# Optimization experiments

Measured on AMD Instinct MI355X. Metric: run time of the kernel, lower is better.

## Reference

```python
import jax, jax.numpy as jnp
import numpy as np

DIM = 512; NH = 8; AG = 144; WIN = 18; PS = 12; B = 128; N0 = 320


def _pool_matrix(in_size, out_size):
    # PyTorch AdaptiveAvgPool2d window rule: start=floor(i*in/out), end=ceil((i+1)*in/out)
    P = np.zeros((out_size, in_size), np.float32)
    for i in range(out_size):
        s = (i * in_size) // out_size
        e = -((-(i + 1) * in_size) // out_size)
        P[i, s:e] = 1.0 / (e - s)
    return jnp.asarray(P)


def setup_inputs() -> dict:
    key = jax.random.key(0)
    ks = jax.random.split(key, 12)
    std = 0.02
    return {
        "x": jax.random.normal(ks[0], (B, N0, DIM), jnp.float32),
        "qkv_w": jax.random.normal(ks[1], (DIM, 3 * DIM), jnp.float32) * 0.02,
        "proj_w": jax.random.normal(ks[2], (DIM, DIM), jnp.float32) * 0.02,
        "proj_b": jnp.zeros((DIM,), jnp.float32),
        "dwc_w": jax.random.normal(ks[3], (DIM, 1, 3, 3), jnp.float32) * 0.1,
        "dwc_b": jnp.zeros((DIM,), jnp.float32),
        "an_bias": jax.random.normal(ks[4], (NH, AG, 7, 7), jnp.float32) * std,
        "na_bias": jax.random.normal(ks[5], (NH, AG, 7, 7), jnp.float32) * std,
        "ah_bias": jax.random.normal(ks[6], (1, NH, AG, WIN, 1), jnp.float32) * std,
        "aw_bias": jax.random.normal(ks[7], (1, NH, AG, 1, WIN), jnp.float32) * std,
        "ha_bias": jax.random.normal(ks[8], (1, NH, WIN, 1, AG), jnp.float32) * std,
        "wa_bias": jax.random.normal(ks[9], (1, NH, 1, WIN, AG), jnp.float32) * std,
    }


def reference(x, qkv_w, proj_w, proj_b, dwc_w, dwc_b,
              an_bias, na_bias, ah_bias, aw_bias, ha_bias, wa_bias):
    b, n0, c = x.shape
    x1 = jnp.pad(x, ((0, 0), (2, 2), (0, 0)))          # pad 2 tokens each side
    n = n0 + 4
    h = w = int(n ** 0.5)
    hd = c // NH
    scale = hd ** -0.5

    qkv = x1 @ qkv_w                                    # (b, n, 3c), no bias
    q, k, v = jnp.split(qkv, 3, axis=-1)

    # agent tokens: adaptive avg pool of q on the (h, w) grid to (PS, PS)
    P = _pool_matrix(h, PS)                             # (12, 18)
    qg = q.reshape(b, h, w, c)
    agent = jnp.einsum('oh,bhwc,pw->bopc', P, qg, P).reshape(b, AG, c)

    def heads(t):
        return t.reshape(b, n, NH, hd).transpose(0, 2, 1, 3)
    q, k, v = heads(q), heads(k), heads(v)              # (b, H, n, hd)
    ag = agent.reshape(b, AG, NH, hd).transpose(0, 2, 1, 3)  # (b, H, A, hd)

    # stage 1: agent <- keys  (ac_bias is concatenated then sliced off => no-op)
    pb1 = jax.image.resize(an_bias, (NH, AG, WIN, WIN), 'bilinear').reshape(1, NH, AG, WIN * WIN)
    pb2 = (ah_bias + aw_bias).reshape(1, NH, AG, WIN * WIN)
    agent_attn = jax.nn.softmax(
        jnp.einsum('bhad,bhnd->bhan', ag * scale, k) + pb1 + pb2, axis=-1)
    agent_v = jnp.einsum('bhan,bhnd->bhad', agent_attn, v)   # (b, H, A, hd)

    # stage 2: queries <- agents (ca_bias sliced off => no-op)
    ab1 = jax.image.resize(na_bias, (NH, AG, WIN, WIN), 'bilinear') \
        .reshape(1, NH, AG, WIN * WIN).transpose(0, 1, 3, 2)  # (1, H, n, A)
    ab2 = (ha_bias + wa_bias).reshape(1, NH, WIN * WIN, AG)
    q_attn = jax.nn.softmax(
        jnp.einsum('bhnd,bhad->bhna', q * scale, ag) + ab1 + ab2, axis=-1)
    out = jnp.einsum('bhna,bhad->bhnd', q_attn, agent_v)
    out = out.transpose(0, 2, 1, 3).reshape(b, n, c)

    # depthwise conv skip on v
    vimg = v.transpose(0, 2, 1, 3).reshape(b, h, w, c).transpose(0, 3, 1, 2)  # (b, c, h, w)
    dwc = jax.lax.conv_general_dilated(vimg, dwc_w, (1, 1), 'SAME',
                                       feature_group_count=c)
    dwc = dwc + dwc_b[None, :, None, None]
    out = out + dwc.transpose(0, 2, 3, 1).reshape(b, n, c)

    out = out @ proj_w + proj_b
    return out[:, 2:-2, :]
```

## Files before the change

kernel.cpp:

```cpp
#include <hip/hip_runtime.h>

typedef unsigned short u16;
typedef short bf16x8 __attribute__((ext_vector_type(8)));
typedef float f32x4 __attribute__((ext_vector_type(4)));

#define B_    128
#define N0_   320
#define C_    512
#define NH_   8
#define HD_   64
#define NTOK  324
#define H_    18
#define AG_   144
#define SCALE 0.125f

typedef __attribute__((address_space(3))) unsigned int as3_u32;
typedef __attribute__((address_space(1))) const unsigned int as1_u32;

__device__ __forceinline__ void gl_lds16(const void* g, void* l) {
  __builtin_amdgcn_global_load_lds((as1_u32*)(unsigned long long)g,
                                   (as3_u32*)(unsigned int)(unsigned long long)l,
                                   16, 0, 0);
}

__device__ __forceinline__ float bfu2f(u16 u) {
  union { unsigned int u; float f; } v; v.u = ((unsigned int)u) << 16; return v.f;
}
__device__ __forceinline__ u16 f2bfu(float f) {
  union { float f; unsigned int u; } v; v.f = f;
  unsigned int r = v.u + 0x7fffu + ((v.u >> 16) & 1u);
  return (u16)(r >> 16);
}

__global__ __launch_bounds__(256) void conv_x(const float* __restrict__ x, u16* __restrict__ xp)
{
  const int idx = blockIdx.x * 256 + threadIdx.x;
  const int row = idx >> 6, c8 = idx & 63;
  const int b = row / NTOK, t = row - b * NTOK;
  u16 o[8];
  if (t < 2 || t >= 322) {
    #pragma unroll
    for (int j = 0; j < 8; ++j) o[j] = 0;
  } else {
    const float* src = x + ((size_t)(b * N0_ + (t - 2))) * C_ + c8 * 8;
    const float4 f0 = *(const float4*)(src);
    const float4 f1 = *(const float4*)(src + 4);
    o[0]=f2bfu(f0.x); o[1]=f2bfu(f0.y); o[2]=f2bfu(f0.z); o[3]=f2bfu(f0.w);
    o[4]=f2bfu(f1.x); o[5]=f2bfu(f1.y); o[6]=f2bfu(f1.z); o[7]=f2bfu(f1.w);
  }
  *(bf16x8*)&xp[(size_t)row * C_ + c8 * 8] = *(bf16x8*)o;
}

__global__ __launch_bounds__(256) void tconv(const float* __restrict__ W, u16* __restrict__ Wt, int ncols)
{
  __shared__ float T[64][65];
  const int k0 = blockIdx.x * 64, n0 = blockIdx.y * 64;
  const int tid = threadIdx.x;
  const int rr = tid >> 4, cc = tid & 15;
  #pragma unroll
  for (int i = 0; i < 4; ++i) {
    const float4 f = *(const float4*)&W[(size_t)(k0 + i * 16 + rr) * ncols + n0 + cc * 4];
    T[i * 16 + rr][cc * 4 + 0] = f.x; T[i * 16 + rr][cc * 4 + 1] = f.y;
    T[i * 16 + rr][cc * 4 + 2] = f.z; T[i * 16 + rr][cc * 4 + 3] = f.w;
  }
  __syncthreads();
  #pragma unroll
  for (int i = 0; i < 4; ++i) {
    const int n = i * 16 + rr;
    ushort4 u;
    u.x = f2bfu(T[cc * 4 + 0][n]); u.y = f2bfu(T[cc * 4 + 1][n]);
    u.z = f2bfu(T[cc * 4 + 2][n]); u.w = f2bfu(T[cc * 4 + 3][n]);
    *(ushort4*)&Wt[(size_t)(n0 + n) * 512 + k0 + cc * 4] = u;
  }
}

template<int MODE>
__global__ __launch_bounds__(256) void mfma_gemm(
    const u16* __restrict__ A, const u16* __restrict__ Bt,
    u16* __restrict__ qb, u16* __restrict__ kb, u16* __restrict__ vb,
    const float* __restrict__ bias, float* __restrict__ outf)
{
  __shared__ __align__(16) u16 As[128 * 64];
  __shared__ __align__(16) u16 Bs[128 * 64];
  const int bx = blockIdx.x;
  const int by = blockIdx.y;
  const int tid = threadIdx.x;
  const int wv = tid >> 6, lane = tid & 63;
  const int lr = lane & 15, lk = lane >> 4;
  const int wr = wv >> 1, wc = wv & 1;
  const int si = lane >> 3, slot = lane & 7;

  size_t arow_src[4];
  #pragma unroll
  for (int jj = 0; jj < 4; ++jj) {
    const int rl = (wv * 4 + jj) * 8 + si;
    const int r = by * 128 + rl;
    if (MODE == 0) {
      arow_src[jj] = (size_t)r * 512;
    } else {
      const int b2 = r / N0_, ii = r - b2 * N0_;
      arow_src[jj] = ((size_t)b2 * 8 * NTOK + (ii + 2)) * 64;
    }
  }

  f32x4 acc[4][4] = {};
  for (int k0 = 0; k0 < 512; k0 += 64) {
    __syncthreads();
    #pragma unroll
    for (int jj = 0; jj < 4; ++jj) {
      const int rl = (wv * 4 + jj) * 8 + si;
      const int c = slot ^ (rl & 7);
      const u16* asrc = (MODE == 0)
          ? (A + arow_src[jj] + k0 + c * 8)
          : (A + arow_src[jj] + (size_t)(k0 >> 6) * (NTOK * 64) + c * 8);
      gl_lds16(asrc, (char*)As + (wv * 4 + jj) * 1024);
      gl_lds16(Bt + (size_t)(bx * 128 + rl) * 512 + k0 + c * 8,
               (char*)Bs + (wv * 4 + jj) * 1024);
    }
    __syncthreads();
    #pragma unroll
    for (int kk = 0; kk < 2; ++kk) {
      bf16x8 af[4], bf[4];
      #pragma unroll
      for (int m = 0; m < 4; ++m) {
        const int row = wr * 64 + m * 16 + lr;
        af[m] = *(const bf16x8*)((const char*)As + row * 128 + (((kk * 4 + lk) ^ (row & 7)) << 4));
      }
      #pragma unroll
      for (int n = 0; n < 4; ++n) {
        const int row = wc * 64 + n * 16 + lr;
        bf[n] = *(const bf16x8*)((const char*)Bs + row * 128 + (((kk * 4 + lk) ^ (row & 7)) << 4));
      }
      #pragma unroll
      for (int m = 0; m < 4; ++m)
        #pragma unroll
        for (int n = 0; n < 4; ++n)
          acc[m][n] = __builtin_amdgcn_mfma_f32_16x16x32_bf16(af[m], bf[n], acc[m][n], 0, 0, 0);
    }
  }

  if (MODE == 0) {
    const int mat = (bx * 128) >> 9;
    u16* outp = (mat == 0) ? qb : (mat == 1) ? kb : vb;
    #pragma unroll
    for (int m = 0; m < 4; ++m) {
      #pragma unroll
      for (int r = 0; r < 4; ++r) {
        const int row = by * 128 + wr * 64 + m * 16 + lk * 4 + r;
        const int b = row / NTOK, t = row - b * NTOK;
        #pragma unroll
        for (int n = 0; n < 4; ++n) {
          const int col = bx * 128 + wc * 64 + n * 16 + lr;
          const int rem = col & 511, h = rem >> 6, d = rem & 63;
          outp[(((size_t)(b * NH_ + h)) * NTOK + t) * HD_ + d] = f2bfu(acc[m][n][r]);
        }
      }
    }
  } else {
    #pragma unroll
    for (int m = 0; m < 4; ++m) {
      #pragma unroll
      for (int r = 0; r < 4; ++r) {
        const int row = by * 128 + wr * 64 + m * 16 + lk * 4 + r;
        #pragma unroll
        for (int n = 0; n < 4; ++n) {
          const int col = bx * 128 + wc * 64 + n * 16 + lr;
          outf[(size_t)row * C_ + col] = acc[m][n][r] + bias[col];
        }
      }
    }
  }
}

__global__ void bias_kernel(const float* __restrict__ an, const float* __restrict__ na,
                            const float* __restrict__ ah, const float* __restrict__ aw,
                            const float* __restrict__ ha, const float* __restrict__ wa,
                            u16* __restrict__ bANT, u16* __restrict__ bNAT)
{
  const int blk = blockIdx.x;
  const int h = blk / AG_, a = blk - h * AG_;
  const int tid = threadIdx.x;
  if (tid >= NTOK) return;
  const int y = tid / H_, x = tid - y * H_;
  float cy = (y + 0.5f) * (7.0f / 18.0f) - 0.5f; cy = fminf(fmaxf(cy, 0.f), 6.f);
  float cx = (x + 0.5f) * (7.0f / 18.0f) - 0.5f; cx = fminf(fmaxf(cx, 0.f), 6.f);
  const int y0 = (int)floorf(cy); const float ty = cy - y0; const int y1 = min(y0 + 1, 6);
  const int x0 = (int)floorf(cx); const float tx = cx - x0; const int x1 = min(x0 + 1, 6);
  const float w00 = (1.f - ty) * (1.f - tx), w01 = (1.f - ty) * tx;
  const float w10 = ty * (1.f - tx), w11 = ty * tx;
  const float* anp = an + (size_t)blk * 49;
  const float* nap = na + (size_t)blk * 49;
  const float van = w00 * anp[y0*7+x0] + w01 * anp[y0*7+x1] + w10 * anp[y1*7+x0] + w11 * anp[y1*7+x1];
  const float vna = w00 * nap[y0*7+x0] + w01 * nap[y0*7+x1] + w10 * nap[y1*7+x0] + w11 * nap[y1*7+x1];
  bANT[((size_t)h * NTOK + tid) * AG_ + a] =
      f2bfu(van + ah[(size_t)blk * H_ + y] + aw[(size_t)blk * H_ + x]);
  bNAT[((size_t)h * AG_ + a) * NTOK + tid] =
      f2bfu(vna + ha[((size_t)h * H_ + y) * AG_ + a] + wa[((size_t)h * H_ + x) * AG_ + a]);
}

__global__ __launch_bounds__(512) void pool_kernel(const u16* __restrict__ qb, u16* __restrict__ agb)
{
  const int blk = blockIdx.x;
  const int b = blk / AG_, a = blk - b * AG_;
  const int o = a / 12, pc = a - o * 12;
  const int y0 = (3 * o) >> 1, x0 = (3 * pc) >> 1;
  const int c = threadIdx.x; const int h = c >> 6, d = c & 63;
  const size_t base = ((size_t)(b * NH_ + h)) * NTOK * HD_ + d;
  const int t00 = (y0 * H_ + x0) * HD_;
  const float v = bfu2f(qb[base + t00]) + bfu2f(qb[base + t00 + HD_])
                + bfu2f(qb[base + t00 + H_ * HD_]) + bfu2f(qb[base + t00 + H_ * HD_ + HD_]);
  agb[((size_t)(b * NH_ + h)) * AG_ * HD_ + a * HD_ + d] = f2bfu(0.25f * v);
}

__global__ __launch_bounds__(512) void dwc_kernel(
    const u16* __restrict__ vb, const float* __restrict__ dwc_w,
    const float* __restrict__ dwc_b, u16* __restrict__ aob)
{
  __shared__ __align__(16) u16 vL[NTOK * 64];
  const int hb = blockIdx.x, h = hb >> 7, b = hb & 127;
  const int bh = b * NH_ + h;
  const int tid = threadIdx.x;
  const bf16x8* vs = (const bf16x8*)(vb + (size_t)bh * NTOK * HD_);
  for (int idx = tid; idx < NTOK * 8; idx += 512)
    ((bf16x8*)vL)[idx] = vs[idx];
  const int d = tid & 63, tg = tid >> 6;
  float w9[9];
  #pragma unroll
  for (int j = 0; j < 9; ++j) w9[j] = dwc_w[(size_t)(h * 64 + d) * 9 + j];
  const float cb = dwc_b[h * 64 + d];
  __syncthreads();
  u16* aout = aob + (size_t)bh * NTOK * HD_;
  for (int t = tg; t < NTOK; t += 8) {
    const int y = t / H_, x = t - y * H_;
    float conv = cb;
    #pragma unroll
    for (int ky = 0; ky < 3; ++ky) {
      const int yy = y + ky - 1;
      if (yy < 0 || yy >= H_) continue;
      #pragma unroll
      for (int kx = 0; kx < 3; ++kx) {
        const int xc = x + kx - 1;
        if (xc < 0 || xc >= H_) continue;
        conv += w9[ky * 3 + kx] * bfu2f(vL[(yy * H_ + xc) * 64 + d]);
      }
    }
    aout[(size_t)t * HD_ + d] = f2bfu(conv);
  }
}

__global__ __launch_bounds__(576) void stage1_k(
    const u16* __restrict__ kb, const u16* __restrict__ vb,
    const u16* __restrict__ agb, const u16* __restrict__ bANT,
    u16* __restrict__ avbT)
{
  __shared__ __align__(16) u16 vT[64 * 360];
  __shared__ __align__(16) u16 pW[9][16][40];
  const int hb = blockIdx.x, h = hb & 7, b = hb >> 3;
  const int bh = b * NH_ + h;
  const int tid = threadIdx.x;
  const int mt = tid >> 6, l = tid & 63, lr = l & 15, lk = l >> 4;

  const u16* vsrc = vb + (size_t)bh * NTOK * HD_;
  for (int idx = tid; idx < 64 * 45; idx += 576) {
    const int d = idx & 63, c = idx >> 6;
    bf16x8 tv;
    #pragma unroll
    for (int j = 0; j < 8; ++j) {
      const int n = c * 8 + j;
      tv[j] = (n < NTOK) ? (short)vsrc[(size_t)n * HD_ + d] : (short)0;
    }
    *(bf16x8*)&vT[d * 360 + c * 8] = tv;
  }

  const u16* aga = agb + ((size_t)bh * AG_ + mt * 16 + lr) * HD_ + lk * 8;
  const bf16x8 a0 = *(const bf16x8*)(aga);
  const bf16x8 a1 = *(const bf16x8*)(aga + 32);

  f32x4 acc[21];
  const u16* kbase = kb + (size_t)bh * NTOK * HD_ + lk * 8;
  __builtin_amdgcn_s_setprio(1);
  #pragma unroll
  for (int nt = 0; nt < 21; ++nt) {
    const bf16x8 b0 = *(const bf16x8*)(kbase + (size_t)(nt * 16 + lr) * HD_);
    const bf16x8 b1 = *(const bf16x8*)(kbase + (size_t)(nt * 16 + lr) * HD_ + 32);
    f32x4 c = {0.f, 0.f, 0.f, 0.f};
    c = __builtin_amdgcn_mfma_f32_16x16x32_bf16(a0, b0, c, 0, 0, 0);
    c = __builtin_amdgcn_mfma_f32_16x16x32_bf16(a1, b1, c, 0, 0, 0);
    acc[nt] = c;
  }
  __builtin_amdgcn_s_setprio(0);

  float mx[4] = {-1e30f, -1e30f, -1e30f, -1e30f};
  #pragma unroll
  for (int nt = 0; nt < 21; ++nt) {
    const int t = nt * 16 + lr;
    const bool valid = (nt < 20) || (lr < 4);
    ushort4 b4 = make_ushort4(0, 0, 0, 0);
    if (valid)
      b4 = *(const ushort4*)&bANT[((size_t)h * NTOK + t) * AG_ + mt * 16 + lk * 4];
    #pragma unroll
    for (int r = 0; r < 4; ++r) {
      float s = -1e30f;
      if (valid) s = acc[nt][r] * SCALE + bfu2f(((const u16*)&b4)[r]);
      acc[nt][r] = s;
      mx[r] = fmaxf(mx[r], s);
    }
  }
  #pragma unroll
  for (int r = 0; r < 4; ++r) {
    #pragma unroll
    for (int o = 1; o < 16; o <<= 1) mx[r] = fmaxf(mx[r], __shfl_xor(mx[r], o));
  }
  float sm[4] = {0.f, 0.f, 0.f, 0.f};
  #pragma unroll
  for (int nt = 0; nt < 21; ++nt) {
    #pragma unroll
    for (int r = 0; r < 4; ++r) {
      const float e = __expf(acc[nt][r] - mx[r]);
      acc[nt][r] = e;
      sm[r] += e;
    }
  }
  #pragma unroll
  for (int r = 0; r < 4; ++r) {
    #pragma unroll
    for (int o = 1; o < 16; o <<= 1) sm[r] += __shfl_xor(sm[r], o);
    sm[r] = 1.0f / sm[r];
  }

  __syncthreads();

  f32x4 ov[4];
  #pragma unroll
  for (int nt2 = 0; nt2 < 4; ++nt2) ov[nt2] = (f32x4){0.f, 0.f, 0.f, 0.f};
  for (int ks = 0; ks < 11; ++ks) {
    #pragma unroll
    for (int half = 0; half < 2; ++half) {
      const int nt = 2 * ks + half;
      #pragma unroll
      for (int r = 0; r < 4; ++r)
        pW[mt][lk * 4 + r][half * 16 + lr] = (nt < 21) ? f2bfu(acc[nt][r] * sm[r]) : (u16)0;
    }
    const bf16x8 pa = *(const bf16x8*)&pW[mt][lr][lk * 8];
    __builtin_amdgcn_s_setprio(1);
    #pragma unroll
    for (int nt2 = 0; nt2 < 4; ++nt2) {
      const bf16x8 vf = *(const bf16x8*)&vT[(nt2 * 16 + lr) * 360 + ks * 32 + lk * 8];
      ov[nt2] = __builtin_amdgcn_mfma_f32_16x16x32_bf16(pa, vf, ov[nt2], 0, 0, 0);
    }
    __builtin_amdgcn_s_setprio(0);
  }

  __syncthreads();

  u16* avTL = vT;
  #pragma unroll
  for (int nt2 = 0; nt2 < 4; ++nt2) {
    ushort4 u;
    u.x = f2bfu(ov[nt2][0]); u.y = f2bfu(ov[nt2][1]);
    u.z = f2bfu(ov[nt2][2]); u.w = f2bfu(ov[nt2][3]);
    *(ushort4*)&avTL[(nt2 * 16 + lr) * 168 + mt * 16 + lk * 4] = u;
  }
  for (int idx = tid; idx < 128; idx += 576)
    *(bf16x8*)&avTL[(idx >> 1) * 168 + 144 + (idx & 1) * 8] = (bf16x8){0,0,0,0,0,0,0,0};

  __syncthreads();

  u16* dst = avbT + (size_t)bh * 64 * 160;
  for (int idx = tid; idx < 64 * 20; idx += 576) {
    const int d = idx / 20, c = idx - d * 20;
    *(bf16x8*)&dst[d * 160 + c * 8] = *(const bf16x8*)&avTL[d * 168 + c * 8];
  }
}

__global__ __launch_bounds__(512, 6) void stage2_k(
    const u16* __restrict__ qb, const u16* __restrict__ agb,
    const u16* __restrict__ avbT, const u16* __restrict__ bNAT,
    u16* __restrict__ aob)
{
  __shared__ __align__(16) u16 avT[64 * 168];
  __shared__ __align__(16) u16 pW[8][16][40];
  __shared__ __align__(16) u16 oB[8][16][72];
  const int hb = blockIdx.x, h = hb & 7, b = hb >> 3;
  const int bh = b * NH_ + h;
  const int tid = threadIdx.x;
  const int wv = tid >> 6, l = tid & 63, lr = l & 15, lk = l >> 4;

  const u16* src = avbT + (size_t)bh * 64 * 160;
  for (int idx = tid; idx < 64 * 20; idx += 512) {
    const int d = idx / 20, c = idx - d * 20;
    *(bf16x8*)&avT[d * 168 + c * 8] = *(const bf16x8*)&src[d * 160 + c * 8];
  }
  __syncthreads();

  u16* aout = aob + (size_t)bh * NTOK * HD_;
  for (int mt2 = wv; mt2 < 21; mt2 += 8) {
    const int arow = min(mt2 * 16 + lr, NTOK - 1);
    const u16* qa = qb + ((size_t)bh * NTOK + arow) * HD_ + lk * 8;
    const bf16x8 qa0 = *(const bf16x8*)(qa);
    const bf16x8 qa1 = *(const bf16x8*)(qa + 32);

    f32x4 acc2[9];
    __builtin_amdgcn_s_setprio(1);
    #pragma unroll
    for (int nt = 0; nt < 9; ++nt) {
      const u16* bp = agb + ((size_t)bh * AG_ + nt * 16 + lr) * HD_ + lk * 8;
      f32x4 c = {0.f, 0.f, 0.f, 0.f};
      c = __builtin_amdgcn_mfma_f32_16x16x32_bf16(qa0, *(const bf16x8*)(bp), c, 0, 0, 0);
      c = __builtin_amdgcn_mfma_f32_16x16x32_bf16(qa1, *(const bf16x8*)(bp + 32), c, 0, 0, 0);
      acc2[nt] = c;
    }
    __builtin_amdgcn_s_setprio(0);

    float mx2[4] = {-1e30f, -1e30f, -1e30f, -1e30f};
    const int t0 = mt2 * 16 + lk * 4;
    #pragma unroll
    for (int nt = 0; nt < 9; ++nt) {
      const ushort4 b4 = *(const ushort4*)&bNAT[((size_t)h * AG_ + nt * 16 + lr) * NTOK + t0];
      #pragma unroll
      for (int r = 0; r < 4; ++r) {
        const float s = acc2[nt][r] * SCALE + bfu2f(((const u16*)&b4)[r]);
        acc2[nt][r] = s;
        mx2[r] = fmaxf(mx2[r], s);
      }
    }
    #pragma unroll
    for (int r = 0; r < 4; ++r) {
      #pragma unroll
      for (int o = 1; o < 16; o <<= 1) mx2[r] = fmaxf(mx2[r], __shfl_xor(mx2[r], o));
    }
    float sm2[4] = {0.f, 0.f, 0.f, 0.f};
    #pragma unroll
    for (int nt = 0; nt < 9; ++nt) {
      #pragma unroll
      for (int r = 0; r < 4; ++r) {
        const float e = __expf(acc2[nt][r] - mx2[r]);
        acc2[nt][r] = e;
        sm2[r] += e;
      }
    }
    #pragma unroll
    for (int r = 0; r < 4; ++r) {
      #pragma unroll
      for (int o = 1; o < 16; o <<= 1) sm2[r] += __shfl_xor(sm2[r], o);
      sm2[r] = 1.0f / sm2[r];
    }

    f32x4 ov2[4];
    #pragma unroll
    for (int dt = 0; dt < 4; ++dt) ov2[dt] = (f32x4){0.f, 0.f, 0.f, 0.f};
    for (int ks = 0; ks < 5; ++ks) {
      #pragma unroll
      for (int half = 0; half < 2; ++half) {
        const int nt = 2 * ks + half;
        #pragma unroll
        for (int r = 0; r < 4; ++r)
          pW[wv][lk * 4 + r][half * 16 + lr] = (nt < 9) ? f2bfu(acc2[nt][r] * sm2[r]) : (u16)0;
      }
      const bf16x8 pa = *(const bf16x8*)&pW[wv][lr][lk * 8];
      __builtin_amdgcn_s_setprio(1);
      #pragma unroll
      for (int dt = 0; dt < 4; ++dt) {
        const bf16x8 vf = *(const bf16x8*)&avT[(dt * 16 + lr) * 168 + ks * 32 + lk * 8];
        ov2[dt] = __builtin_amdgcn_mfma_f32_16x16x32_bf16(vf, pa, ov2[dt], 0, 0, 0);
      }
      __builtin_amdgcn_s_setprio(0);
    }

    #pragma unroll
    for (int dt = 0; dt < 4; ++dt) {
      ushort4 u;
      u.x = f2bfu(ov2[dt][0]); u.y = f2bfu(ov2[dt][1]);
      u.z = f2bfu(ov2[dt][2]); u.w = f2bfu(ov2[dt][3]);
      *(ushort4*)&oB[wv][lr][dt * 16 + lk * 4] = u;
    }
    const int tloc = l >> 2, part = l & 3;
    if (mt2 * 16 + tloc < NTOK) {
      u16* gp = &aout[(size_t)(mt2 * 16 + tloc) * HD_ + part * 16];
      const u16* lp = &oB[wv][tloc][part * 16];
      const bf16x8 g0 = *(const bf16x8*)(gp);
      const bf16x8 g1 = *(const bf16x8*)(gp + 8);
      const bf16x8 l0 = *(const bf16x8*)(lp);
      const bf16x8 l1 = *(const bf16x8*)(lp + 8);
      bf16x8 o0, o1;
      #pragma unroll
      for (int j = 0; j < 8; ++j) {
        o0[j] = (short)f2bfu(bfu2f((u16)g0[j]) + bfu2f((u16)l0[j]));
        o1[j] = (short)f2bfu(bfu2f((u16)g1[j]) + bfu2f((u16)l1[j]));
      }
      *(bf16x8*)(gp) = o0;
      *(bf16x8*)(gp + 8) = o1;
    }
  }
}

extern "C" void kernel_launch(void* const* d_in, const int* in_sizes, int n_in,
                              void* d_out, int out_size, void* d_ws, size_t ws_size,
                              hipStream_t stream)
{
  (void)in_sizes; (void)n_in; (void)out_size;
  const float* x      = (const float*)d_in[0];
  const float* qkv_w  = (const float*)d_in[1];
  const float* proj_w = (const float*)d_in[2];
  const float* proj_b = (const float*)d_in[3];
  const float* dwc_w  = (const float*)d_in[4];
  const float* dwc_b  = (const float*)d_in[5];
  const float* an     = (const float*)d_in[6];
  const float* na     = (const float*)d_in[7];
  const float* ah     = (const float*)d_in[8];
  const float* aw     = (const float*)d_in[9];
  const float* ha     = (const float*)d_in[10];
  const float* wa     = (const float*)d_in[11];

  char* ws = (char*)d_ws;
  const size_t QB   = (size_t)B_ * NH_ * NTOK * HD_ * 2;
  const size_t AGB  = (size_t)B_ * NH_ * AG_  * HD_ * 2;
  const size_t AVTB = (size_t)B_ * NH_ * 64 * 160 * 2;
  const size_t BB   = (size_t)NH_ * AG_ * NTOK * 2 + 64;
  const size_t WQ   = (size_t)1536 * 512 * 2;
  const size_t WP   = (size_t)512 * 512 * 2;
  u16* qb    = (u16*)(ws);
  u16* kb    = (u16*)(ws + QB);
  u16* vb    = (u16*)(ws + 2 * QB);
  u16* xp    = (u16*)(ws + 3 * QB);
  u16* agb   = (u16*)(ws + 3 * QB);
  u16* avbT  = (u16*)(ws + 3 * QB + AGB);
  u16* bANT  = (u16*)(ws + 3 * QB + AGB + AVTB);
  u16* wqkvT = (u16*)(ws + 4 * QB);
  u16* wprojT= (u16*)(ws + 4 * QB + WQ);
  u16* bNAT  = (u16*)(ws + 4 * QB + WQ + WP);
  u16* aob   = kb;
  if (ws_size < 4 * QB + WQ + WP + BB) return;

  conv_x   <<<dim3(B_ * NTOK * 64 / 256), dim3(256), 0, stream>>>(x, xp);
  tconv    <<<dim3(8, 24), dim3(256), 0, stream>>>(qkv_w, wqkvT, 1536);
  tconv    <<<dim3(8, 8),  dim3(256), 0, stream>>>(proj_w, wprojT, 512);
  mfma_gemm<0><<<dim3(12, 324), dim3(256), 0, stream>>>(xp, wqkvT, qb, kb, vb, nullptr, nullptr);
  pool_kernel<<<dim3(B_ * AG_),  dim3(512), 0, stream>>>(qb, agb);
  bias_kernel<<<dim3(NH_ * AG_), dim3(324), 0, stream>>>(an, na, ah, aw, ha, wa, bANT, bNAT);
  stage1_k <<<dim3(NH_ * B_), dim3(576), 0, stream>>>(kb, vb, agb, bANT, avbT);
  dwc_kernel<<<dim3(NH_ * B_), dim3(512), 0, stream>>>(vb, dwc_w, dwc_b, aob);
  stage2_k <<<dim3(NH_ * B_), dim3(512), 0, stream>>>(qb, agb, avbT, bNAT, aob);
  mfma_gemm<1><<<dim3(4, 320), dim3(256), 0, stream>>>(aob, wprojT, nullptr, nullptr, nullptr, proj_b, (float*)d_out);
}
```

Baseline: 487.9 us.

## Vectorize GEMM epilogue stores and process two batches per attention block

The GEMM swaps the MFMA operand order so each lane holds four consecutive columns, which lets the epilogue write ushort4/float4 vectors instead of scalar stores for both the QKV scatter and the projection output. Separately, the stage1 and stage2 attention kernels now loop over two batch entries per block and launch half as many blocks. This amortizes block launch cost but gives fewer blocks for latency hiding and adds extra syncs between the two iterations.

```diff
diff --git a/kernel.cpp b/kernel.cpp
--- a/kernel.cpp
+++ b/kernel.cpp
@@ -135,7 +135,7 @@
       for (int m = 0; m < 4; ++m)
         #pragma unroll
         for (int n = 0; n < 4; ++n)
-          acc[m][n] = __builtin_amdgcn_mfma_f32_16x16x32_bf16(af[m], bf[n], acc[m][n], 0, 0, 0);
+          acc[m][n] = __builtin_amdgcn_mfma_f32_16x16x32_bf16(bf[n], af[m], acc[m][n], 0, 0, 0);
     }
   }
 
@@ -144,29 +144,31 @@
     u16* outp = (mat == 0) ? qb : (mat == 1) ? kb : vb;
     #pragma unroll
     for (int m = 0; m < 4; ++m) {
-      #pragma unroll
-      for (int r = 0; r < 4; ++r) {
-        const int row = by * 128 + wr * 64 + m * 16 + lk * 4 + r;
-        const int b = row / NTOK, t = row - b * NTOK;
-        #pragma unroll
-        for (int n = 0; n < 4; ++n) {
-          const int col = bx * 128 + wc * 64 + n * 16 + lr;
-          const int rem = col & 511, h = rem >> 6, d = rem & 63;
-          outp[(((size_t)(b * NH_ + h)) * NTOK + t) * HD_ + d] = f2bfu(acc[m][n][r]);
-        }
+      const int row = by * 128 + wr * 64 + m * 16 + lr;
+      const int b = row / NTOK, t = row - b * NTOK;
+      #pragma unroll
+      for (int n = 0; n < 4; ++n) {
+        const int col = bx * 128 + wc * 64 + n * 16 + lk * 4;
+        const int rem = col & 511, h = rem >> 6, d = rem & 63;
+        ushort4 u;
+        u.x = f2bfu(acc[m][n][0]); u.y = f2bfu(acc[m][n][1]);
+        u.z = f2bfu(acc[m][n][2]); u.w = f2bfu(acc[m][n][3]);
+        *(ushort4*)&outp[(((size_t)(b * NH_ + h)) * NTOK + t) * HD_ + d] = u;
       }
     }
   } else {
     #pragma unroll
     for (int m = 0; m < 4; ++m) {
-      #pragma unroll
-      for (int r = 0; r < 4; ++r) {
-        const int row = by * 128 + wr * 64 + m * 16 + lk * 4 + r;
-        #pragma unroll
-        for (int n = 0; n < 4; ++n) {
-          const int col = bx * 128 + wc * 64 + n * 16 + lr;
-          outf[(size_t)row * C_ + col] = acc[m][n][r] + bias[col];
-        }
+      const int row = by * 128 + wr * 64 + m * 16 + lr;
+      #pragma unroll
+      for (int n = 0; n < 4; ++n) {
+        const int col = bx * 128 + wc * 64 + n * 16 + lk * 4;
+        float4 o;
+        o.x = acc[m][n][0] + bias[col + 0];
+        o.y = acc[m][n][1] + bias[col + 1];
+        o.z = acc[m][n][2] + bias[col + 2];
+        o.w = acc[m][n][3] + bias[col + 3];
+        *(float4*)&outf[(size_t)row * C_ + col] = o;
       }
     }
   }
@@ -255,121 +257,125 @@
 {
   __shared__ __align__(16) u16 vT[64 * 360];
   __shared__ __align__(16) u16 pW[9][16][40];
-  const int hb = blockIdx.x, h = hb & 7, b = hb >> 3;
-  const int bh = b * NH_ + h;
+  const int hb = blockIdx.x, h = hb & 7, bbase = (hb >> 3) * 2;
   const int tid = threadIdx.x;
   const int mt = tid >> 6, l = tid & 63, lr = l & 15, lk = l >> 4;
 
-  const u16* vsrc = vb + (size_t)bh * NTOK * HD_;
-  for (int idx = tid; idx < 64 * 45; idx += 576) {
-    const int d = idx & 63, c = idx >> 6;
-    bf16x8 tv;
-    #pragma unroll
-    for (int j = 0; j < 8; ++j) {
-      const int n = c * 8 + j;
-      tv[j] = (n < NTOK) ? (short)vsrc[(size_t)n * HD_ + d] : (short)0;
-    }
-    *(bf16x8*)&vT[d * 360 + c * 8] = tv;
-  }
-
-  const u16* aga = agb + ((size_t)bh * AG_ + mt * 16 + lr) * HD_ + lk * 8;
-  const bf16x8 a0 = *(const bf16x8*)(aga);
-  const bf16x8 a1 = *(const bf16x8*)(aga + 32);
-
-  f32x4 acc[21];
-  const u16* kbase = kb + (size_t)bh * NTOK * HD_ + lk * 8;
-  __builtin_amdgcn_s_setprio(1);
-  #pragma unroll
-  for (int nt = 0; nt < 21; ++nt) {
-    const bf16x8 b0 = *(const bf16x8*)(kbase + (size_t)(nt * 16 + lr) * HD_);
-    const bf16x8 b1 = *(const bf16x8*)(kbase + (size_t)(nt * 16 + lr) * HD_ + 32);
-    f32x4 c = {0.f, 0.f, 0.f, 0.f};
-    c = __builtin_amdgcn_mfma_f32_16x16x32_bf16(a0, b0, c, 0, 0, 0);
-    c = __builtin_amdgcn_mfma_f32_16x16x32_bf16(a1, b1, c, 0, 0, 0);
-    acc[nt] = c;
-  }
-  __builtin_amdgcn_s_setprio(0);
-
-  float mx[4] = {-1e30f, -1e30f, -1e30f, -1e30f};
-  #pragma unroll
-  for (int nt = 0; nt < 21; ++nt) {
-    const int t = nt * 16 + lr;
-    const bool valid = (nt < 20) || (lr < 4);
-    ushort4 b4 = make_ushort4(0, 0, 0, 0);
-    if (valid)
-      b4 = *(const ushort4*)&bANT[((size_t)h * NTOK + t) * AG_ + mt * 16 + lk * 4];
+  for (int bb2 = 0; bb2 < 2; ++bb2) {
+    const int bh = (bbase + bb2) * NH_ + h;
+
+    const u16* vsrc = vb + (size_t)bh * NTOK * HD_;
+    for (int idx = tid; idx < 64 * 45; idx += 576) {
+      const int d = idx & 63, c = idx >> 6;
+      bf16x8 tv;
+      #pragma unroll
+      for (int j = 0; j < 8; ++j) {
+        const int n = c * 8 + j;
+        tv[j] = (n < NTOK) ? (short)vsrc[(size_t)n * HD_ + d] : (short)0;
+      }
+      *(bf16x8*)&vT[d * 360 + c * 8] = tv;
+    }
+
+    const u16* aga = agb + ((size_t)bh * AG_ + mt * 16 + lr) * HD_ + lk * 8;
+    const bf16x8 a0 = *(const bf16x8*)(aga);
+    const bf16x8 a1 = *(const bf16x8*)(aga + 32);
+
+    f32x4 acc[21];
+    const u16* kbase = kb + (size_t)bh * NTOK * HD_ + lk * 8;
+    __builtin_amdgcn_s_setprio(1);
+    #pragma unroll
+    for (int nt = 0; nt < 21; ++nt) {
+      const bf16x8 b0 = *(const bf16x8*)(kbase + (size_t)(nt * 16 + lr) * HD_);
+      const bf16x8 b1 = *(const bf16x8*)(kbase + (size_t)(nt * 16 + lr) * HD_ + 32);
+      f32x4 c = {0.f, 0.f, 0.f, 0.f};
+      c = __builtin_amdgcn_mfma_f32_16x16x32_bf16(a0, b0, c, 0, 0, 0);
+      c = __builtin_amdgcn_mfma_f32_16x16x32_bf16(a1, b1, c, 0, 0, 0);
+      acc[nt] = c;
+    }
+    __builtin_amdgcn_s_setprio(0);
+
+    float mx[4] = {-1e30f, -1e30f, -1e30f, -1e30f};
+    #pragma unroll
+    for (int nt = 0; nt < 21; ++nt) {
+      const int t = nt * 16 + lr;
+      const bool valid = (nt < 20) || (lr < 4);
+      ushort4 b4 = make_ushort4(0, 0, 0, 0);
+      if (valid)
+        b4 = *(const ushort4*)&bANT[((size_t)h * NTOK + t) * AG_ + mt * 16 + lk * 4];
+      #pragma unroll
+      for (int r = 0; r < 4; ++r) {
+        float s = -1e30f;
+        if (valid) s = acc[nt][r] * SCALE + bfu2f(((const u16*)&b4)[r]);
+        acc[nt][r] = s;
+        mx[r] = fmaxf(mx[r], s);
+      }
+    }
     #pragma unroll
     for (int r = 0; r < 4; ++r) {
-      float s = -1e30f;
-      if (valid) s = acc[nt][r] * SCALE + bfu2f(((const u16*)&b4)[r]);
-      acc[nt][r] = s;
-      mx[r] = fmaxf(mx[r], s);
-    }
-  }
-  #pragma unroll
-  for (int r = 0; r < 4; ++r) {
-    #pragma unroll
-    for (int o = 1; o < 16; o <<= 1) mx[r] = fmaxf(mx[r], __shfl_xor(mx[r], o));
-  }
-  float sm[4] = {0.f, 0.f, 0.f, 0.f};
-  #pragma unroll
-  for (int nt = 0; nt < 21; ++nt) {
+      #pragma unroll
+      for (int o = 1; o < 16; o <<= 1) mx[r] = fmaxf(mx[r], __shfl_xor(mx[r], o));
+    }
+    float sm[4] = {0.f, 0.f, 0.f, 0.f};
+    #pragma unroll
+    for (int nt = 0; nt < 21; ++nt) {
+      #pragma unroll
+      for (int r = 0; r < 4; ++r) {
+        const float e = __expf(acc[nt][r] - mx[r]);
+        acc[nt][r] = e;
+        sm[r] += e;
+      }
+    }
     #pragma unroll
     for (int r = 0; r < 4; ++r) {
-      const float e = __expf(acc[nt][r] - mx[r]);
-      acc[nt][r] = e;
-      sm[r] += e;
-    }
-  }
-  #pragma unroll
-  for (int r = 0; r < 4; ++r) {
-    #pragma unroll
-    for (int o = 1; o < 16; o <<= 1) sm[r] += __shfl_xor(sm[r], o);
-    sm[r] = 1.0f / sm[r];
-  }
-
-  __syncthreads();
-
-  f32x4 ov[4];
-  #pragma unroll
-  for (int nt2 = 0; nt2 < 4; ++nt2) ov[nt2] = (f32x4){0.f, 0.f, 0.f, 0.f};
-  for (int ks = 0; ks < 11; ++ks) {
-    #pragma unroll
-    for (int half = 0; half < 2; ++half) {
-      const int nt = 2 * ks + half;
-      #pragma unroll
-      for (int r = 0; r < 4; ++r)
-        pW[mt][lk * 4 + r][half * 16 + lr] = (nt < 21) ? f2bfu(acc[nt][r] * sm[r]) : (u16)0;
-    }
-    const bf16x8 pa = *(const bf16x8*)&pW[mt][lr][lk * 8];
-    __builtin_amdgcn_s_setprio(1);
+      #pragma unroll
+      for (int o = 1; o < 16; o <<= 1) sm[r] += __shfl_xor(sm[r], o);
+      sm[r] = 1.0f / sm[r];
+    }
+
+    __syncthreads();
+
+    f32x4 ov[4];
+    #pragma unroll
+    for (int nt2 = 0; nt2 < 4; ++nt2) ov[nt2] = (f32x4){0.f, 0.f, 0.f, 0.f};
+    for (int ks = 0; ks < 11; ++ks) {
+      #pragma unroll
+      for (int half = 0; half < 2; ++half) {
+        const int nt = 2 * ks + half;
+        #pragma unroll
+        for (int r = 0; r < 4; ++r)
+          pW[mt][lk * 4 + r][half * 16 + lr] = (nt < 21) ? f2bfu(acc[nt][r] * sm[r]) : (u16)0;
+      }
+      const bf16x8 pa = *(const bf16x8*)&pW[mt][lr][lk * 8];
+      __builtin_amdgcn_s_setprio(1);
+      #pragma unroll
+      for (int nt2 = 0; nt2 < 4; ++nt2) {
+        const bf16x8 vf = *(const bf16x8*)&vT[(nt2 * 16 + lr) * 360 + ks * 32 + lk * 8];
+        ov[nt2] = __builtin_amdgcn_mfma_f32_16x16x32_bf16(pa, vf, ov[nt2], 0, 0, 0);
+      }
+      __builtin_amdgcn_s_setprio(0);
+    }
+
+    __syncthreads();
+
+    u16* avTL = vT;
     #pragma unroll
     for (int nt2 = 0; nt2 < 4; ++nt2) {
-      const bf16x8 vf = *(const bf16x8*)&vT[(nt2 * 16 + lr) * 360 + ks * 32 + lk * 8];
-      ov[nt2] = __builtin_amdgcn_mfma_f32_16x16x32_bf16(pa, vf, ov[nt2], 0, 0, 0);
-    }
-    __builtin_amdgcn_s_setprio(0);
-  }
-
-  __syncthreads();
-
-  u16* avTL = vT;
-  #pragma unroll
-  for (int nt2 = 0; nt2 < 4; ++nt2) {
-    ushort4 u;
-    u.x = f2bfu(ov[nt2][0]); u.y = f2bfu(ov[nt2][1]);
-    u.z = f2bfu(ov[nt2][2]); u.w = f2bfu(ov[nt2][3]);
-    *(ushort4*)&avTL[(nt2 * 16 + lr) * 168 + mt * 16 + lk * 4] = u;
-  }
-  for (int idx = tid; idx < 128; idx += 576)
-    *(bf16x8*)&avTL[(idx >> 1) * 168 + 144 + (idx & 1) * 8] = (bf16x8){0,0,0,0,0,0,0,0};
-
-  __syncthreads();
-
-  u16* dst = avbT + (size_t)bh * 64 * 160;
-  for (int idx = tid; idx < 64 * 20; idx += 576) {
-    const int d = idx / 20, c = idx - d * 20;
-    *(bf16x8*)&dst[d * 160 + c * 8] = *(const bf16x8*)&avTL[d * 168 + c * 8];
+      ushort4 u;
+      u.x = f2bfu(ov[nt2][0]); u.y = f2bfu(ov[nt2][1]);
+      u.z = f2bfu(ov[nt2][2]); u.w = f2bfu(ov[nt2][3]);
+      *(ushort4*)&avTL[(nt2 * 16 + lr) * 168 + mt * 16 + lk * 4] = u;
+    }
+    for (int idx = tid; idx < 128; idx += 576)
+      *(bf16x8*)&avTL[(idx >> 1) * 168 + 144 + (idx & 1) * 8] = (bf16x8){0,0,0,0,0,0,0,0};
+
+    __syncthreads();
+
+    u16* dst = avbT + (size_t)bh * 64 * 160;
+    for (int idx = tid; idx < 64 * 20; idx += 576) {
+      const int d = idx / 20, c = idx - d * 20;
+      *(bf16x8*)&dst[d * 160 + c * 8] = *(const bf16x8*)&avTL[d * 168 + c * 8];
+    }
+    __syncthreads();
   }
 }
 
@@ -381,116 +387,120 @@
   __shared__ __align__(16) u16 avT[64 * 168];
   __shared__ __align__(16) u16 pW[8][16][40];
   __shared__ __align__(16) u16 oB[8][16][72];
-  const int hb = blockIdx.x, h = hb & 7, b = hb >> 3;
-  const int bh = b * NH_ + h;
+  const int hb = blockIdx.x, h = hb & 7, bbase = (hb >> 3) * 2;
   const int tid = threadIdx.x;
   const int wv = tid >> 6, l = tid & 63, lr = l & 15, lk = l >> 4;
 
-  const u16* src = avbT + (size_t)bh * 64 * 160;
-  for (int idx = tid; idx < 64 * 20; idx += 512) {
-    const int d = idx / 20, c = idx - d * 20;
-    *(bf16x8*)&avT[d * 168 + c * 8] = *(const bf16x8*)&src[d * 160 + c * 8];
-  }
-  __syncthreads();
-
-  u16* aout = aob + (size_t)bh * NTOK * HD_;
-  for (int mt2 = wv; mt2 < 21; mt2 += 8) {
-    const int arow = min(mt2 * 16 + lr, NTOK - 1);
-    const u16* qa = qb + ((size_t)bh * NTOK + arow) * HD_ + lk * 8;
-    const bf16x8 qa0 = *(const bf16x8*)(qa);
-    const bf16x8 qa1 = *(const bf16x8*)(qa + 32);
-
-    f32x4 acc2[9];
-    __builtin_amdgcn_s_setprio(1);
-    #pragma unroll
-    for (int nt = 0; nt < 9; ++nt) {
-      const u16* bp = agb + ((size_t)bh * AG_ + nt * 16 + lr) * HD_ + lk * 8;
-      f32x4 c = {0.f, 0.f, 0.f, 0.f};
-      c = __builtin_amdgcn_mfma_f32_16x16x32_bf16(qa0, *(const bf16x8*)(bp), c, 0, 0, 0);
-      c = __builtin_amdgcn_mfma_f32_16x16x32_bf16(qa1, *(const bf16x8*)(bp + 32), c, 0, 0, 0);
-      acc2[nt] = c;
-    }
-    __builtin_amdgcn_s_setprio(0);
-
-    float mx2[4] = {-1e30f, -1e30f, -1e30f, -1e30f};
-    const int t0 = mt2 * 16 + lk * 4;
-    #pragma unroll
-    for (int nt = 0; nt < 9; ++nt) {
-      const ushort4 b4 = *(const ushort4*)&bNAT[((size_t)h * AG_ + nt * 16 + lr) * NTOK + t0];
+  for (int bb2 = 0; bb2 < 2; ++bb2) {
+    const int bh = (bbase + bb2) * NH_ + h;
+
+    const u16* src = avbT + (size_t)bh * 64 * 160;
+    for (int idx = tid; idx < 64 * 20; idx += 512) {
+      const int d = idx / 20, c = idx - d * 20;
+      *(bf16x8*)&avT[d * 168 + c * 8] = *(const bf16x8*)&src[d * 160 + c * 8];
+    }
+    __syncthreads();
+
+    u16* aout = aob + (size_t)bh * NTOK * HD_;
+    for (int mt2 = wv; mt2 < 21; mt2 += 8) {
+      const int arow = min(mt2 * 16 + lr, NTOK - 1);
+      const u16* qa = qb + ((size_t)bh * NTOK + arow) * HD_ + lk * 8;
+      const bf16x8 qa0 = *(const bf16x8*)(qa);
+      const bf16x8 qa1 = *(const bf16x8*)(qa + 32);
+
+      f32x4 acc2[9];
+      __builtin_amdgcn_s_setprio(1);
+      #pragma unroll
+      for (int nt = 0; nt < 9; ++nt) {
+        const u16* bp = agb + ((size_t)bh * AG_ + nt * 16 + lr) * HD_ + lk * 8;
+        f32x4 c = {0.f, 0.f, 0.f, 0.f};
+        c = __builtin_amdgcn_mfma_f32_16x16x32_bf16(qa0, *(const bf16x8*)(bp), c, 0, 0, 0);
+        c = __builtin_amdgcn_mfma_f32_16x16x32_bf16(qa1, *(const bf16x8*)(bp + 32), c, 0, 0, 0);
+        acc2[nt] = c;
+      }
+      __builtin_amdgcn_s_setprio(0);
+
+      float mx2[4] = {-1e30f, -1e30f, -1e30f, -1e30f};
+      const int t0 = mt2 * 16 + lk * 4;
+      #pragma unroll
+      for (int nt = 0; nt < 9; ++nt) {
+        const ushort4 b4 = *(const ushort4*)&bNAT[((size_t)h * AG_ + nt * 16 + lr) * NTOK + t0];
+        #pragma unroll
+        for (int r = 0; r < 4; ++r) {
+          const float s = acc2[nt][r] * SCALE + bfu2f(((const u16*)&b4)[r]);
+          acc2[nt][r] = s;
+          mx2[r] = fmaxf(mx2[r], s);
+        }
+      }
       #pragma unroll
       for (int r = 0; r < 4; ++r) {
-        const float s = acc2[nt][r] * SCALE + bfu2f(((const u16*)&b4)[r]);
-        acc2[nt][r] = s;
-        mx2[r] = fmaxf(mx2[r], s);
-      }
-    }
-    #pragma unroll
-    for (int r = 0; r < 4; ++r) {
-      #pragma unroll
-      for (int o = 1; o < 16; o <<= 1) mx2[r] = fmaxf(mx2[r], __shfl_xor(mx2[r], o));
-    }
-    float sm2[4] = {0.f, 0.f, 0.f, 0.f};
-    #pragma unroll
-    for (int nt = 0; nt < 9; ++nt) {
+        #pragma unroll
+        for (int o = 1; o < 16; o <<= 1) mx2[r] = fmaxf(mx2[r], __shfl_xor(mx2[r], o));
+      }
+      float sm2[4] = {0.f, 0.f, 0.f, 0.f};
+      #pragma unroll
+      for (int nt = 0; nt < 9; ++nt) {
+        #pragma unroll
+        for (int r = 0; r < 4; ++r) {
+          const float e = __expf(acc2[nt][r] - mx2[r]);
+          acc2[nt][r] = e;
+          sm2[r] += e;
+        }
+      }
       #pragma unroll
       for (int r = 0; r < 4; ++r) {
-        const float e = __expf(acc2[nt][r] - mx2[r]);
-        acc2[nt][r] = e;
-        sm2[r] += e;
-      }
-    }
-    #pragma unroll
-    for (int r = 0; r < 4; ++r) {
-      #pragma unroll
-      for (int o = 1; o < 16; o <<= 1) sm2[r] += __shfl_xor(sm2[r], o);
-      sm2[r] = 1.0f / sm2[r];
-    }
-
-    f32x4 ov2[4];
-    #pragma unroll
-    for (int dt = 0; dt < 4; ++dt) ov2[dt] = (f32x4){0.f, 0.f, 0.f, 0.f};
-    for (int ks = 0; ks < 5; ++ks) {
-      #pragma unroll
-      for (int half = 0; half < 2; ++half) {
-        const int nt = 2 * ks + half;
-        #pragma unroll
-        for (int r = 0; r < 4; ++r)
-          pW[wv][lk * 4 + r][half * 16 + lr] = (nt < 9) ? f2bfu(acc2[nt][r] * sm2[r]) : (u16)0;
-      }
-      const bf16x8 pa = *(const bf16x8*)&pW[wv][lr][lk * 8];
-      __builtin_amdgcn_s_setprio(1);
+        #pragma unroll
+        for (int o = 1; o < 16; o <<= 1) sm2[r] += __shfl_xor(sm2[r], o);
+        sm2[r] = 1.0f / sm2[r];
+      }
+
+      f32x4 ov2[4];
+      #pragma unroll
+      for (int dt = 0; dt < 4; ++dt) ov2[dt] = (f32x4){0.f, 0.f, 0.f, 0.f};
+      for (int ks = 0; ks < 5; ++ks) {
+        #pragma unroll
+        for (int half = 0; half < 2; ++half) {
+          const int nt = 2 * ks + half;
+          #pragma unroll
+          for (int r = 0; r < 4; ++r)
+            pW[wv][lk * 4 + r][half * 16 + lr] = (nt < 9) ? f2bfu(acc2[nt][r] * sm2[r]) : (u16)0;
+        }
+        const bf16x8 pa = *(const bf16x8*)&pW[wv][lr][lk * 8];
+        __builtin_amdgcn_s_setprio(1);
+        #pragma unroll
+        for (int dt = 0; dt < 4; ++dt) {
+          const bf16x8 vf = *(const bf16x8*)&avT[(dt * 16 + lr) * 168 + ks * 32 + lk * 8];
+          ov2[dt] = __builtin_amdgcn_mfma_f32_16x16x32_bf16(vf, pa, ov2[dt], 0, 0, 0);
+        }
+        __builtin_amdgcn_s_setprio(0);
+      }
+
       #pragma unroll
       for (int dt = 0; dt < 4; ++dt) {
-        const bf16x8 vf = *(const bf16x8*)&avT[(dt * 16 + lr) * 168 + ks * 32 + lk * 8];
-        ov2[dt] = __builtin_amdgcn_mfma_f32_16x16x32_bf16(vf, pa, ov2[dt], 0, 0, 0);
-      }
-      __builtin_amdgcn_s_setprio(0);
-    }
-
-    #pragma unroll
-    for (int dt = 0; dt < 4; ++dt) {
-      ushort4 u;
-      u.x = f2bfu(ov2[dt][0]); u.y = f2bfu(ov2[dt][1]);
-      u.z = f2bfu(ov2[dt][2]); u.w = f2bfu(ov2[dt][3]);
-      *(ushort4*)&oB[wv][lr][dt * 16 + lk * 4] = u;
-    }
-    const int tloc = l >> 2, part = l & 3;
-    if (mt2 * 16 + tloc < NTOK) {
-      u16* gp = &aout[(size_t)(mt2 * 16 + tloc) * HD_ + part * 16];
-      const u16* lp = &oB[wv][tloc][part * 16];
-      const bf16x8 g0 = *(const bf16x8*)(gp);
-      const bf16x8 g1 = *(const bf16x8*)(gp + 8);
-      const bf16x8 l0 = *(const bf16x8*)(lp);
-      const bf16x8 l1 = *(const bf16x8*)(lp + 8);
-      bf16x8 o0, o1;
-      #pragma unroll
-      for (int j = 0; j < 8; ++j) {
-        o0[j] = (short)f2bfu(bfu2f((u16)g0[j]) + bfu2f((u16)l0[j]));
-        o1[j] = (short)f2bfu(bfu2f((u16)g1[j]) + bfu2f((u16)l1[j]));
-      }
-      *(bf16x8*)(gp) = o0;
-      *(bf16x8*)(gp + 8) = o1;
-    }
+        ushort4 u;
+        u.x = f2bfu(ov2[dt][0]); u.y = f2bfu(ov2[dt][1]);
+        u.z = f2bfu(ov2[dt][2]); u.w = f2bfu(ov2[dt][3]);
+        *(ushort4*)&oB[wv][lr][dt * 16 + lk * 4] = u;
+      }
+      const int tloc = l >> 2, part = l & 3;
+      if (mt2 * 16 + tloc < NTOK) {
+        u16* gp = &aout[(size_t)(mt2 * 16 + tloc) * HD_ + part * 16];
+        const u16* lp = &oB[wv][tloc][part * 16];
+        const bf16x8 g0 = *(const bf16x8*)(gp);
+        const bf16x8 g1 = *(const bf16x8*)(gp + 8);
+        const bf16x8 l0 = *(const bf16x8*)(lp);
+        const bf16x8 l1 = *(const bf16x8*)(lp + 8);
+        bf16x8 o0, o1;
+        #pragma unroll
+        for (int j = 0; j < 8; ++j) {
+          o0[j] = (short)f2bfu(bfu2f((u16)g0[j]) + bfu2f((u16)l0[j]));
+          o1[j] = (short)f2bfu(bfu2f((u16)g1[j]) + bfu2f((u16)l1[j]));
+        }
+        *(bf16x8*)(gp) = o0;
+        *(bf16x8*)(gp + 8) = o1;
+      }
+    }
+    __syncthreads();
   }
 }
 
@@ -538,8 +548,8 @@
   mfma_gemm<0><<<dim3(12, 324), dim3(256), 0, stream>>>(xp, wqkvT, qb, kb, vb, nullptr, nullptr);
   pool_kernel<<<dim3(B_ * AG_),  dim3(512), 0, stream>>>(qb, agb);
   bias_kernel<<<dim3(NH_ * AG_), dim3(324), 0, stream>>>(an, na, ah, aw, ha, wa, bANT, bNAT);
-  stage1_k <<<dim3(NH_ * B_), dim3(576), 0, stream>>>(kb, vb, agb, bANT, avbT);
+  stage1_k <<<dim3(NH_ * B_ / 2), dim3(576), 0, stream>>>(kb, vb, agb, bANT, avbT);
   dwc_kernel<<<dim3(NH_ * B_), dim3(512), 0, stream>>>(vb, dwc_w, dwc_b, aob);
-  stage2_k <<<dim3(NH_ * B_), dim3(512), 0, stream>>>(qb, agb, avbT, bNAT, aob);
+  stage2_k <<<dim3(NH_ * B_ / 2), dim3(512), 0, stream>>>(qb, agb, avbT, bNAT, aob);
   mfma_gemm<1><<<dim3(4, 320), dim3(256), 0, stream>>>(aob, wprojT, nullptr, nullptr, nullptr, proj_b, (float*)d_out);
 }
```

After: 531.0 us. +8.8%, slower.
